# Kernel tuning notes

Measured on AMD Instinct MI355X. Metric: run time of the kernel, lower is better.

## Reference

```python
import jax, jax.numpy as jnp
import numpy as np

N = 50000   # n_nodes
E = 800000  # n_edges (avg degree 16)
D = 128     # d_model == hidden_dim
N_LAYERS = 3


def _xavier(key, fan_in, fan_out):
    limit = float(np.sqrt(6.0 / (fan_in + fan_out)))
    return jax.random.uniform(key, (fan_in, fan_out), jnp.float32, -limit, limit)


def setup_inputs() -> dict:
    key = jax.random.key(0)
    ks = jax.random.split(key, 2 + 2 * N_LAYERS)
    x = jax.random.normal(ks[0], (N, D), jnp.float32)
    edge_index = jax.random.randint(ks[1], (2, E), 0, N, jnp.int32)
    inp = {"x": x, "edge_index": edge_index}
    for i in range(N_LAYERS):
        inp[f"W{i}"] = _xavier(ks[2 + 2 * i], D, D)
        inp[f"b{i}"] = jax.random.uniform(ks[3 + 2 * i], (D,), jnp.float32, -0.1, 0.1)
    return inp


def _gcn_forward(x, src, dst, norm, Ws, bs):
    n = x.shape[0]
    h = x
    for i, (W, b) in enumerate(zip(Ws, bs)):
        m = (h @ W)[src] * norm[:, None]                       # [E+N, D] gather + scale
        h = jax.ops.segment_sum(m, dst, num_segments=n) + b    # scatter-add aggregate
        if i < len(Ws) - 1:
            h = jax.nn.relu(h)
    return h + x                                               # residual


def reference(x, edge_index, W0, b0, W1, b1, W2, b2):
    n = x.shape[0]
    loop = jnp.arange(n, dtype=edge_index.dtype)
    src = jnp.concatenate([edge_index[0], loop])  # add self-loops (GCNConv default)
    dst = jnp.concatenate([edge_index[1], loop])
    deg = jax.ops.segment_sum(jnp.ones_like(dst, x.dtype), dst, num_segments=n)
    dinv = jax.lax.rsqrt(deg)                     # deg >= 1 due to self-loops
    norm = dinv[src] * dinv[dst]                  # symmetric GCN normalization
    return _gcn_forward(x, src, dst, norm, (W0, W1, W2), (b0, b1, b2))
```

## Files before the change

kernel.cpp:

```cpp
#include <hip/hip_runtime.h>
#include <hip/hip_bf16.h>

#define D 128
#define BCAP 64
#define TM 64
#define TMF 32


__device__ __forceinline__ unsigned short f2bf_rtne(float f) {
    unsigned int u = __float_as_uint(f);
    u += 0x7fffu + ((u >> 16) & 1u);
    return (unsigned short)(u >> 16);
}

__device__ __forceinline__ float bf_lo(unsigned int u) { return __uint_as_float(u << 16); }
__device__ __forceinline__ float bf_hi(unsigned int u) { return __uint_as_float(u & 0xffff0000u); }


__device__ __forceinline__ void gemm_compute64(const float* __restrict__ sh,
                                               const float* __restrict__ W,
                                               unsigned short* __restrict__ out,
                                               const int* __restrict__ cnt,
                                               int n, int nbase) {
    const int tid = threadIdx.x;
    const int c4 = (tid & 31) << 2;
    const int ng = tid >> 5;
    const float* shb = &sh[(ng * 8) * D];

    float4 acc[8];
#pragma unroll
    for (int j = 0; j < 8; ++j) acc[j] = make_float4(0.f, 0.f, 0.f, 0.f);

    for (int k = 0; k < D; k += 4) {
        float4 w0 = *(const float4*)&W[(size_t)(k + 0) * D + c4];
        float4 w1 = *(const float4*)&W[(size_t)(k + 1) * D + c4];
        float4 w2 = *(const float4*)&W[(size_t)(k + 2) * D + c4];
        float4 w3 = *(const float4*)&W[(size_t)(k + 3) * D + c4];
#pragma unroll
        for (int j = 0; j < 8; ++j) {
            float4 hv = *(const float4*)&shb[j * D + k];
            acc[j].x = fmaf(hv.x, w0.x, acc[j].x); acc[j].y = fmaf(hv.x, w0.y, acc[j].y);
            acc[j].z = fmaf(hv.x, w0.z, acc[j].z); acc[j].w = fmaf(hv.x, w0.w, acc[j].w);
            acc[j].x = fmaf(hv.y, w1.x, acc[j].x); acc[j].y = fmaf(hv.y, w1.y, acc[j].y);
            acc[j].z = fmaf(hv.y, w1.z, acc[j].z); acc[j].w = fmaf(hv.y, w1.w, acc[j].w);
            acc[j].x = fmaf(hv.z, w2.x, acc[j].x); acc[j].y = fmaf(hv.z, w2.y, acc[j].y);
            acc[j].z = fmaf(hv.z, w2.z, acc[j].z); acc[j].w = fmaf(hv.z, w2.w, acc[j].w);
            acc[j].x = fmaf(hv.w, w3.x, acc[j].x); acc[j].y = fmaf(hv.w, w3.y, acc[j].y);
            acc[j].z = fmaf(hv.w, w3.z, acc[j].z); acc[j].w = fmaf(hv.w, w3.w, acc[j].w);
        }
    }

#pragma unroll
    for (int j = 0; j < 8; ++j) {
        int node = nbase + ng * 8 + j;
        if (node < n) {
            float sc = 1.0f;
            if (cnt) sc = rsqrtf((float)cnt[node] + 1.0f);
            ushort4 p;
            p.x = f2bf_rtne(acc[j].x * sc);
            p.y = f2bf_rtne(acc[j].y * sc);
            p.z = f2bf_rtne(acc[j].z * sc);
            p.w = f2bf_rtne(acc[j].w * sc);
            *(ushort4*)&out[(size_t)node * D + c4] = p;
        }
    }
}


__global__ __launch_bounds__(256) void fused_gemm0_fill_kernel(
        const float* __restrict__ x, const float* __restrict__ W0,
        unsigned short* __restrict__ A,
        const int* __restrict__ src, const int* __restrict__ dst,
        int* __restrict__ cnt, unsigned short* __restrict__ bucket,
        int n, int E, int r, int gemmB, int fillB) {
    __shared__ float sh[TMF * D];
    int b = blockIdx.x;
    if (b % r == 0) {
        int g = b / r;
        if (g >= gemmB) return;
        const int tid = threadIdx.x;
        const int nbase = g * TMF;
#pragma unroll
        for (int i = 0; i < 4; ++i) {
            int fi = tid + i * 256;
            int node = nbase + (fi >> 5);
            float4 v = make_float4(0.f, 0.f, 0.f, 0.f);
            if (node < n) v = *(const float4*)&x[(size_t)node * D + ((fi & 31) << 2)];
            *(float4*)&sh[fi << 2] = v;
        }
        __syncthreads();

        const int c4 = (tid & 31) << 2;
        const int ng = tid >> 5;
        const float* shb = &sh[(ng * 4) * D];
        float4 acc[4];
#pragma unroll
        for (int j = 0; j < 4; ++j) acc[j] = make_float4(0.f, 0.f, 0.f, 0.f);

        for (int k = 0; k < D; k += 4) {
            float4 w0 = *(const float4*)&W0[(size_t)(k + 0) * D + c4];
            float4 w1 = *(const float4*)&W0[(size_t)(k + 1) * D + c4];
            float4 w2 = *(const float4*)&W0[(size_t)(k + 2) * D + c4];
            float4 w3 = *(const float4*)&W0[(size_t)(k + 3) * D + c4];
#pragma unroll
            for (int j = 0; j < 4; ++j) {
                float4 hv = *(const float4*)&shb[j * D + k];
                acc[j].x = fmaf(hv.x, w0.x, acc[j].x); acc[j].y = fmaf(hv.x, w0.y, acc[j].y);
                acc[j].z = fmaf(hv.x, w0.z, acc[j].z); acc[j].w = fmaf(hv.x, w0.w, acc[j].w);
                acc[j].x = fmaf(hv.y, w1.x, acc[j].x); acc[j].y = fmaf(hv.y, w1.y, acc[j].y);
                acc[j].z = fmaf(hv.y, w1.z, acc[j].z); acc[j].w = fmaf(hv.y, w1.w, acc[j].w);
                acc[j].x = fmaf(hv.z, w2.x, acc[j].x); acc[j].y = fmaf(hv.z, w2.y, acc[j].y);
                acc[j].z = fmaf(hv.z, w2.z, acc[j].z); acc[j].w = fmaf(hv.z, w2.w, acc[j].w);
                acc[j].x = fmaf(hv.w, w3.x, acc[j].x); acc[j].y = fmaf(hv.w, w3.y, acc[j].y);
                acc[j].z = fmaf(hv.w, w3.z, acc[j].z); acc[j].w = fmaf(hv.w, w3.w, acc[j].w);
            }
        }

#pragma unroll
        for (int j = 0; j < 4; ++j) {
            int node = nbase + ng * 4 + j;
            if (node < n) {
                ushort4 p;
                p.x = f2bf_rtne(acc[j].x);
                p.y = f2bf_rtne(acc[j].y);
                p.z = f2bf_rtne(acc[j].z);
                p.w = f2bf_rtne(acc[j].w);
                *(ushort4*)&A[(size_t)node * D + c4] = p;
            }
        }
    } else {
        int fid = b - b / r - 1;
        if (fid >= fillB) return;
        int e = fid * 256 + threadIdx.x;
        if (e >= E) return;
        int s = src[e];
        int d = dst[e];
        int pos = atomicAdd(&cnt[d], 1);
        if (pos < BCAP) bucket[((size_t)d << 6) + pos] = (unsigned short)s;
    }
}


__global__ __launch_bounds__(256) void gemm128_scaled_kernel(
        const unsigned short* __restrict__ h, const float* __restrict__ W,
        unsigned short* __restrict__ out, const int* __restrict__ cnt, int n) {
    __shared__ float sh[TM * D];
    const int tid = threadIdx.x;
    const int nbase = blockIdx.x * TM;
#pragma unroll
    for (int i = 0; i < 8; ++i) {
        int fi = tid + i * 256;
        int node = nbase + (fi >> 5);
        float4 v = make_float4(0.f, 0.f, 0.f, 0.f);
        if (node < n) {
            ushort4 u = *(const ushort4*)&h[(size_t)node * D + ((fi & 31) << 2)];
            v.x = __uint_as_float((unsigned)u.x << 16);
            v.y = __uint_as_float((unsigned)u.y << 16);
            v.z = __uint_as_float((unsigned)u.z << 16);
            v.w = __uint_as_float((unsigned)u.w << 16);
        }
        *(float4*)&sh[fi << 2] = v;
    }
    __syncthreads();
    gemm_compute64(sh, W, out, cnt, n, nbase);
}


__global__ __launch_bounds__(256) void gather_kernel(
        const int* __restrict__ cnt, const unsigned short* __restrict__ bucket,
        const unsigned short* __restrict__ hW, const float* __restrict__ bias,
        const float* __restrict__ x, float* __restrict__ out_f32,
        unsigned short* __restrict__ out_bf16, int n, int scaled_in, int final_layer) {
    int node = blockIdx.x * 8 + (threadIdx.x >> 5);
    if (node >= n) return;
    const int f = (threadIdx.x & 31) << 2;
    const unsigned short* row = bucket + ((size_t)node << 6);
    int len = cnt[node];
    float di = rsqrtf((float)len + 1.0f);
    if (len > BCAP) len = BCAP;
    const int len8 = len & ~7;

    float4 acc0 = make_float4(0.f, 0.f, 0.f, 0.f);
    float4 acc1 = make_float4(0.f, 0.f, 0.f, 0.f);
    int k = 0;
    if (len8 > 0) {
        uint4 pp = *(const uint4*)row;
        if (scaled_in) {
            for (; k < len8; k += 8) {
                uint4 cur = pp;
                pp = *(const uint4*)(row + k + 8);
                int s0 = cur.x & 0xffff, s1 = cur.x >> 16;
                int s2 = cur.y & 0xffff, s3 = cur.y >> 16;
                int s4 = cur.z & 0xffff, s5 = cur.z >> 16;
                int s6 = cur.w & 0xffff, s7 = cur.w >> 16;
                uint2 u0 = *(const uint2*)&hW[(size_t)s0 * D + f];
                uint2 u1 = *(const uint2*)&hW[(size_t)s1 * D + f];
                uint2 u2 = *(const uint2*)&hW[(size_t)s2 * D + f];
                uint2 u3 = *(const uint2*)&hW[(size_t)s3 * D + f];
                uint2 u4 = *(const uint2*)&hW[(size_t)s4 * D + f];
                uint2 u5 = *(const uint2*)&hW[(size_t)s5 * D + f];
                uint2 u6 = *(const uint2*)&hW[(size_t)s6 * D + f];
                uint2 u7 = *(const uint2*)&hW[(size_t)s7 * D + f];
                acc0.x += bf_lo(u0.x); acc0.y += bf_hi(u0.x); acc0.z += bf_lo(u0.y); acc0.w += bf_hi(u0.y);
                acc1.x += bf_lo(u1.x); acc1.y += bf_hi(u1.x); acc1.z += bf_lo(u1.y); acc1.w += bf_hi(u1.y);
                acc0.x += bf_lo(u2.x); acc0.y += bf_hi(u2.x); acc0.z += bf_lo(u2.y); acc0.w += bf_hi(u2.y);
                acc1.x += bf_lo(u3.x); acc1.y += bf_hi(u3.x); acc1.z += bf_lo(u3.y); acc1.w += bf_hi(u3.y);
                acc0.x += bf_lo(u4.x); acc0.y += bf_hi(u4.x); acc0.z += bf_lo(u4.y); acc0.w += bf_hi(u4.y);
                acc1.x += bf_lo(u5.x); acc1.y += bf_hi(u5.x); acc1.z += bf_lo(u5.y); acc1.w += bf_hi(u5.y);
                acc0.x += bf_lo(u6.x); acc0.y += bf_hi(u6.x); acc0.z += bf_lo(u6.y); acc0.w += bf_hi(u6.y);
                acc1.x += bf_lo(u7.x); acc1.y += bf_hi(u7.x); acc1.z += bf_lo(u7.y); acc1.w += bf_hi(u7.y);
            }
        } else {
            for (; k < len8; k += 8) {
                uint4 cur = pp;
                pp = *(const uint4*)(row + k + 8);
                int s0 = cur.x & 0xffff, s1 = cur.x >> 16;
                int s2 = cur.y & 0xffff, s3 = cur.y >> 16;
                int s4 = cur.z & 0xffff, s5 = cur.z >> 16;
                int s6 = cur.w & 0xffff, s7 = cur.w >> 16;
                float n0 = rsqrtf((float)cnt[s0] + 1.0f);
                float n1 = rsqrtf((float)cnt[s1] + 1.0f);
                float n2 = rsqrtf((float)cnt[s2] + 1.0f);
                float n3 = rsqrtf((float)cnt[s3] + 1.0f);
                float n4 = rsqrtf((float)cnt[s4] + 1.0f);
                float n5 = rsqrtf((float)cnt[s5] + 1.0f);
                float n6 = rsqrtf((float)cnt[s6] + 1.0f);
                float n7 = rsqrtf((float)cnt[s7] + 1.0f);
                uint2 u0 = *(const uint2*)&hW[(size_t)s0 * D + f];
                uint2 u1 = *(const uint2*)&hW[(size_t)s1 * D + f];
                uint2 u2 = *(const uint2*)&hW[(size_t)s2 * D + f];
                uint2 u3 = *(const uint2*)&hW[(size_t)s3 * D + f];
                uint2 u4 = *(const uint2*)&hW[(size_t)s4 * D + f];
                uint2 u5 = *(const uint2*)&hW[(size_t)s5 * D + f];
                uint2 u6 = *(const uint2*)&hW[(size_t)s6 * D + f];
                uint2 u7 = *(const uint2*)&hW[(size_t)s7 * D + f];
                acc0.x = fmaf(bf_lo(u0.x), n0, acc0.x); acc0.y = fmaf(bf_hi(u0.x), n0, acc0.y);
                acc0.z = fmaf(bf_lo(u0.y), n0, acc0.z); acc0.w = fmaf(bf_hi(u0.y), n0, acc0.w);
                acc1.x = fmaf(bf_lo(u1.x), n1, acc1.x); acc1.y = fmaf(bf_hi(u1.x), n1, acc1.y);
                acc1.z = fmaf(bf_lo(u1.y), n1, acc1.z); acc1.w = fmaf(bf_hi(u1.y), n1, acc1.w);
                acc0.x = fmaf(bf_lo(u2.x), n2, acc0.x); acc0.y = fmaf(bf_hi(u2.x), n2, acc0.y);
                acc0.z = fmaf(bf_lo(u2.y), n2, acc0.z); acc0.w = fmaf(bf_hi(u2.y), n2, acc0.w);
                acc1.x = fmaf(bf_lo(u3.x), n3, acc1.x); acc1.y = fmaf(bf_hi(u3.x), n3, acc1.y);
                acc1.z = fmaf(bf_lo(u3.y), n3, acc1.z); acc1.w = fmaf(bf_hi(u3.y), n3, acc1.w);
                acc0.x = fmaf(bf_lo(u4.x), n4, acc0.x); acc0.y = fmaf(bf_hi(u4.x), n4, acc0.y);
                acc0.z = fmaf(bf_lo(u4.y), n4, acc0.z); acc0.w = fmaf(bf_hi(u4.y), n4, acc0.w);
                acc1.x = fmaf(bf_lo(u5.x), n5, acc1.x); acc1.y = fmaf(bf_hi(u5.x), n5, acc1.y);
                acc1.z = fmaf(bf_lo(u5.y), n5, acc1.z); acc1.w = fmaf(bf_hi(u5.y), n5, acc1.w);
                acc0.x = fmaf(bf_lo(u6.x), n6, acc0.x); acc0.y = fmaf(bf_hi(u6.x), n6, acc0.y);
                acc0.z = fmaf(bf_lo(u6.y), n6, acc0.z); acc0.w = fmaf(bf_hi(u6.y), n6, acc0.w);
                acc1.x = fmaf(bf_lo(u7.x), n7, acc1.x); acc1.y = fmaf(bf_hi(u7.x), n7, acc1.y);
                acc1.z = fmaf(bf_lo(u7.y), n7, acc1.z); acc1.w = fmaf(bf_hi(u7.y), n7, acc1.w);
            }
        }
    }
    for (; k < len; ++k) {
        int s = row[k];
        float ns = scaled_in ? 1.0f : rsqrtf((float)cnt[s] + 1.0f);
        uint2 u = *(const uint2*)&hW[(size_t)s * D + f];
        acc0.x = fmaf(bf_lo(u.x), ns, acc0.x); acc0.y = fmaf(bf_hi(u.x), ns, acc0.y);
        acc0.z = fmaf(bf_lo(u.y), ns, acc0.z); acc0.w = fmaf(bf_hi(u.y), ns, acc0.w);
    }

    uint2 uh = *(const uint2*)&hW[(size_t)node * D + f];
    float sf = scaled_in ? 1.0f : di;
    float4 acc;
    acc.x = fmaf(bf_lo(uh.x), sf, acc0.x + acc1.x);
    acc.y = fmaf(bf_hi(uh.x), sf, acc0.y + acc1.y);
    acc.z = fmaf(bf_lo(uh.y), sf, acc0.z + acc1.z);
    acc.w = fmaf(bf_hi(uh.y), sf, acc0.w + acc1.w);

    float4 bv = *(const float4*)&bias[f];
    float4 r;
    r.x = fmaf(acc.x, di, bv.x);
    r.y = fmaf(acc.y, di, bv.y);
    r.z = fmaf(acc.z, di, bv.z);
    r.w = fmaf(acc.w, di, bv.w);

    if (final_layer) {
        float4 xv = *(const float4*)&x[(size_t)node * D + f];
        r.x += xv.x; r.y += xv.y; r.z += xv.z; r.w += xv.w;
        *(float4*)&out_f32[(size_t)node * D + f] = r;
    } else {
        ushort4 p;
        p.x = f2bf_rtne(fmaxf(r.x, 0.f));
        p.y = f2bf_rtne(fmaxf(r.y, 0.f));
        p.z = f2bf_rtne(fmaxf(r.z, 0.f));
        p.w = f2bf_rtne(fmaxf(r.w, 0.f));
        *(ushort4*)&out_bf16[(size_t)node * D + f] = p;
    }
}


extern "C" void kernel_launch(void* const* d_in, const int* in_sizes, int n_in,
                              void* d_out, int out_size, void* d_ws, size_t ws_size,
                              hipStream_t stream) {
    const float* x  = (const float*)d_in[0];
    const int*   ei = (const int*)d_in[1];
    const float* Ws[3] = {(const float*)d_in[2], (const float*)d_in[4], (const float*)d_in[6]};
    const float* bs[3] = {(const float*)d_in[3], (const float*)d_in[5], (const float*)d_in[7]};
    float* out = (float*)d_out;

    const int N = in_sizes[0] / D;
    const int E = in_sizes[1] / 2;
    const int* src = ei;
    const int* dst = ei + E;

    char* wsb = (char*)d_ws;
    size_t off = 0;
    int* cnt = (int*)(wsb + off);               off += (size_t)N * sizeof(int);
    off = (off + 255) & ~(size_t)255;
    unsigned short* bucket = (unsigned short*)(wsb + off);  off += (size_t)N * BCAP * 2;
    off = (off + 255) & ~(size_t)255;
    unsigned short* A  = (unsigned short*)(wsb + off);      off += (size_t)N * D * 2;
    off = (off + 255) & ~(size_t)255;
    unsigned short* B  = (unsigned short*)(wsb + off);

    const int gemmBF = (N + TMF - 1) / TMF;
    const int gemmB  = (N + TM - 1) / TM;
    const int fillB = (E + 255) / 256;
    const int r = 1 + (fillB + gemmBF - 1) / gemmBF;
    const int fusedGrid = gemmBF * r;
    const int gatherGrid = (N + 7) / 8;

    hipMemsetAsync(cnt, 0, (size_t)N * sizeof(int), stream);
    fused_gemm0_fill_kernel<<<fusedGrid, 256, 0, stream>>>(x, Ws[0], A, src, dst,
                                                           cnt, bucket, N, E, r, gemmBF, fillB);
    gather_kernel<<<gatherGrid, 256, 0, stream>>>(cnt, bucket, A, bs[0], x, out, B, N, 0, 0);
    gemm128_scaled_kernel<<<gemmB, 256, 0, stream>>>(B, Ws[1], A, cnt, N);
    gather_kernel<<<gatherGrid, 256, 0, stream>>>(cnt, bucket, A, bs[1], x, out, B, N, 1, 0);
    gemm128_scaled_kernel<<<gemmB, 256, 0, stream>>>(B, Ws[2], A, cnt, N);
    gather_kernel<<<gatherGrid, 256, 0, stream>>>(cnt, bucket, A, bs[2], x, out, B, N, 1, 1);
}
```

Baseline: 325.3 us.

## Fuse neighbor aggregation with next-layer GEMM and enlarge first GEMM tile

Layer 0 and 1 aggregation now writes the activated rows of 32 nodes into shared memory and multiplies them by the next weight matrix in the same kernel. This removes the bf16 intermediate round trip through global memory and two kernel launches. It double-buffers the hW arrays (A/A2) because a block reads gathered neighbor rows from other blocks. The first fused GEMM+fill kernel also goes from 32 to 64 nodes per GEMM block. In exchange, the fused kernel has fewer threads gathering per node-tile and may have different occupancy from the extra shared memory.

```diff
diff --git a/kernel.cpp b/kernel.cpp
--- a/kernel.cpp
+++ b/kernel.cpp
@@ -4,7 +4,7 @@
 #define D 128
 #define BCAP 64
 #define TM 64
-#define TMF 32
+#define TG 32
 
 
 __device__ __forceinline__ unsigned short f2bf_rtne(float f) {
@@ -17,163 +17,11 @@
 __device__ __forceinline__ float bf_hi(unsigned int u) { return __uint_as_float(u & 0xffff0000u); }
 
 
-__device__ __forceinline__ void gemm_compute64(const float* __restrict__ sh,
-                                               const float* __restrict__ W,
-                                               unsigned short* __restrict__ out,
-                                               const int* __restrict__ cnt,
-                                               int n, int nbase) {
-    const int tid = threadIdx.x;
-    const int c4 = (tid & 31) << 2;
-    const int ng = tid >> 5;
-    const float* shb = &sh[(ng * 8) * D];
-
-    float4 acc[8];
-#pragma unroll
-    for (int j = 0; j < 8; ++j) acc[j] = make_float4(0.f, 0.f, 0.f, 0.f);
-
-    for (int k = 0; k < D; k += 4) {
-        float4 w0 = *(const float4*)&W[(size_t)(k + 0) * D + c4];
-        float4 w1 = *(const float4*)&W[(size_t)(k + 1) * D + c4];
-        float4 w2 = *(const float4*)&W[(size_t)(k + 2) * D + c4];
-        float4 w3 = *(const float4*)&W[(size_t)(k + 3) * D + c4];
-#pragma unroll
-        for (int j = 0; j < 8; ++j) {
-            float4 hv = *(const float4*)&shb[j * D + k];
-            acc[j].x = fmaf(hv.x, w0.x, acc[j].x); acc[j].y = fmaf(hv.x, w0.y, acc[j].y);
-            acc[j].z = fmaf(hv.x, w0.z, acc[j].z); acc[j].w = fmaf(hv.x, w0.w, acc[j].w);
-            acc[j].x = fmaf(hv.y, w1.x, acc[j].x); acc[j].y = fmaf(hv.y, w1.y, acc[j].y);
-            acc[j].z = fmaf(hv.y, w1.z, acc[j].z); acc[j].w = fmaf(hv.y, w1.w, acc[j].w);
-            acc[j].x = fmaf(hv.z, w2.x, acc[j].x); acc[j].y = fmaf(hv.z, w2.y, acc[j].y);
-            acc[j].z = fmaf(hv.z, w2.z, acc[j].z); acc[j].w = fmaf(hv.z, w2.w, acc[j].w);
-            acc[j].x = fmaf(hv.w, w3.x, acc[j].x); acc[j].y = fmaf(hv.w, w3.y, acc[j].y);
-            acc[j].z = fmaf(hv.w, w3.z, acc[j].z); acc[j].w = fmaf(hv.w, w3.w, acc[j].w);
-        }
-    }
-
-#pragma unroll
-    for (int j = 0; j < 8; ++j) {
-        int node = nbase + ng * 8 + j;
-        if (node < n) {
-            float sc = 1.0f;
-            if (cnt) sc = rsqrtf((float)cnt[node] + 1.0f);
-            ushort4 p;
-            p.x = f2bf_rtne(acc[j].x * sc);
-            p.y = f2bf_rtne(acc[j].y * sc);
-            p.z = f2bf_rtne(acc[j].z * sc);
-            p.w = f2bf_rtne(acc[j].w * sc);
-            *(ushort4*)&out[(size_t)node * D + c4] = p;
-        }
-    }
-}
-
-
-__global__ __launch_bounds__(256) void fused_gemm0_fill_kernel(
-        const float* __restrict__ x, const float* __restrict__ W0,
-        unsigned short* __restrict__ A,
-        const int* __restrict__ src, const int* __restrict__ dst,
-        int* __restrict__ cnt, unsigned short* __restrict__ bucket,
-        int n, int E, int r, int gemmB, int fillB) {
-    __shared__ float sh[TMF * D];
-    int b = blockIdx.x;
-    if (b % r == 0) {
-        int g = b / r;
-        if (g >= gemmB) return;
-        const int tid = threadIdx.x;
-        const int nbase = g * TMF;
-#pragma unroll
-        for (int i = 0; i < 4; ++i) {
-            int fi = tid + i * 256;
-            int node = nbase + (fi >> 5);
-            float4 v = make_float4(0.f, 0.f, 0.f, 0.f);
-            if (node < n) v = *(const float4*)&x[(size_t)node * D + ((fi & 31) << 2)];
-            *(float4*)&sh[fi << 2] = v;
-        }
-        __syncthreads();
-
-        const int c4 = (tid & 31) << 2;
-        const int ng = tid >> 5;
-        const float* shb = &sh[(ng * 4) * D];
-        float4 acc[4];
-#pragma unroll
-        for (int j = 0; j < 4; ++j) acc[j] = make_float4(0.f, 0.f, 0.f, 0.f);
-
-        for (int k = 0; k < D; k += 4) {
-            float4 w0 = *(const float4*)&W0[(size_t)(k + 0) * D + c4];
-            float4 w1 = *(const float4*)&W0[(size_t)(k + 1) * D + c4];
-            float4 w2 = *(const float4*)&W0[(size_t)(k + 2) * D + c4];
-            float4 w3 = *(const float4*)&W0[(size_t)(k + 3) * D + c4];
-#pragma unroll
-            for (int j = 0; j < 4; ++j) {
-                float4 hv = *(const float4*)&shb[j * D + k];
-                acc[j].x = fmaf(hv.x, w0.x, acc[j].x); acc[j].y = fmaf(hv.x, w0.y, acc[j].y);
-                acc[j].z = fmaf(hv.x, w0.z, acc[j].z); acc[j].w = fmaf(hv.x, w0.w, acc[j].w);
-                acc[j].x = fmaf(hv.y, w1.x, acc[j].x); acc[j].y = fmaf(hv.y, w1.y, acc[j].y);
-                acc[j].z = fmaf(hv.y, w1.z, acc[j].z); acc[j].w = fmaf(hv.y, w1.w, acc[j].w);
-                acc[j].x = fmaf(hv.z, w2.x, acc[j].x); acc[j].y = fmaf(hv.z, w2.y, acc[j].y);
-                acc[j].z = fmaf(hv.z, w2.z, acc[j].z); acc[j].w = fmaf(hv.z, w2.w, acc[j].w);
-                acc[j].x = fmaf(hv.w, w3.x, acc[j].x); acc[j].y = fmaf(hv.w, w3.y, acc[j].y);
-                acc[j].z = fmaf(hv.w, w3.z, acc[j].z); acc[j].w = fmaf(hv.w, w3.w, acc[j].w);
-            }
-        }
-
-#pragma unroll
-        for (int j = 0; j < 4; ++j) {
-            int node = nbase + ng * 4 + j;
-            if (node < n) {
-                ushort4 p;
-                p.x = f2bf_rtne(acc[j].x);
-                p.y = f2bf_rtne(acc[j].y);
-                p.z = f2bf_rtne(acc[j].z);
-                p.w = f2bf_rtne(acc[j].w);
-                *(ushort4*)&A[(size_t)node * D + c4] = p;
-            }
-        }
-    } else {
-        int fid = b - b / r - 1;
-        if (fid >= fillB) return;
-        int e = fid * 256 + threadIdx.x;
-        if (e >= E) return;
-        int s = src[e];
-        int d = dst[e];
-        int pos = atomicAdd(&cnt[d], 1);
-        if (pos < BCAP) bucket[((size_t)d << 6) + pos] = (unsigned short)s;
-    }
-}
-
-
-__global__ __launch_bounds__(256) void gemm128_scaled_kernel(
-        const unsigned short* __restrict__ h, const float* __restrict__ W,
-        unsigned short* __restrict__ out, const int* __restrict__ cnt, int n) {
-    __shared__ float sh[TM * D];
-    const int tid = threadIdx.x;
-    const int nbase = blockIdx.x * TM;
-#pragma unroll
-    for (int i = 0; i < 8; ++i) {
-        int fi = tid + i * 256;
-        int node = nbase + (fi >> 5);
-        float4 v = make_float4(0.f, 0.f, 0.f, 0.f);
-        if (node < n) {
-            ushort4 u = *(const ushort4*)&h[(size_t)node * D + ((fi & 31) << 2)];
-            v.x = __uint_as_float((unsigned)u.x << 16);
-            v.y = __uint_as_float((unsigned)u.y << 16);
-            v.z = __uint_as_float((unsigned)u.z << 16);
-            v.w = __uint_as_float((unsigned)u.w << 16);
-        }
-        *(float4*)&sh[fi << 2] = v;
-    }
-    __syncthreads();
-    gemm_compute64(sh, W, out, cnt, n, nbase);
-}
-
-
-__global__ __launch_bounds__(256) void gather_kernel(
-        const int* __restrict__ cnt, const unsigned short* __restrict__ bucket,
-        const unsigned short* __restrict__ hW, const float* __restrict__ bias,
-        const float* __restrict__ x, float* __restrict__ out_f32,
-        unsigned short* __restrict__ out_bf16, int n, int scaled_in, int final_layer) {
-    int node = blockIdx.x * 8 + (threadIdx.x >> 5);
-    if (node >= n) return;
-    const int f = (threadIdx.x & 31) << 2;
+__device__ __forceinline__ float4 aggregate_row(const int* __restrict__ cnt,
+                                                const unsigned short* __restrict__ bucket,
+                                                const unsigned short* __restrict__ hW,
+                                                const float* __restrict__ bias,
+                                                int node, int f, int scaled_in) {
     const unsigned short* row = bucket + ((size_t)node << 6);
     int len = cnt[node];
     float di = rsqrtf((float)len + 1.0f);
@@ -275,19 +123,163 @@
     r.y = fmaf(acc.y, di, bv.y);
     r.z = fmaf(acc.z, di, bv.z);
     r.w = fmaf(acc.w, di, bv.w);
-
-    if (final_layer) {
-        float4 xv = *(const float4*)&x[(size_t)node * D + f];
-        r.x += xv.x; r.y += xv.y; r.z += xv.z; r.w += xv.w;
-        *(float4*)&out_f32[(size_t)node * D + f] = r;
+    return r;
+}
+
+
+__global__ __launch_bounds__(256) void fused_gemm0_fill_kernel(
+        const float* __restrict__ x, const float* __restrict__ W0,
+        unsigned short* __restrict__ A,
+        const int* __restrict__ src, const int* __restrict__ dst,
+        int* __restrict__ cnt, unsigned short* __restrict__ bucket,
+        int n, int E, int r, int gemmB, int fillB) {
+    __shared__ float sh[TM * D];
+    int b = blockIdx.x;
+    if (b % r == 0) {
+        int g = b / r;
+        if (g >= gemmB) return;
+        const int tid = threadIdx.x;
+        const int nbase = g * TM;
+#pragma unroll
+        for (int i = 0; i < 8; ++i) {
+            int fi = tid + i * 256;
+            int node = nbase + (fi >> 5);
+            float4 v = make_float4(0.f, 0.f, 0.f, 0.f);
+            if (node < n) v = *(const float4*)&x[(size_t)node * D + ((fi & 31) << 2)];
+            *(float4*)&sh[fi << 2] = v;
+        }
+        __syncthreads();
+
+        const int c4 = (tid & 31) << 2;
+        const int ng = tid >> 5;
+        const float* shb = &sh[(ng * 8) * D];
+        float4 acc[8];
+#pragma unroll
+        for (int j = 0; j < 8; ++j) acc[j] = make_float4(0.f, 0.f, 0.f, 0.f);
+
+        for (int k = 0; k < D; k += 4) {
+            float4 w0 = *(const float4*)&W0[(size_t)(k + 0) * D + c4];
+            float4 w1 = *(const float4*)&W0[(size_t)(k + 1) * D + c4];
+            float4 w2 = *(const float4*)&W0[(size_t)(k + 2) * D + c4];
+            float4 w3 = *(const float4*)&W0[(size_t)(k + 3) * D + c4];
+#pragma unroll
+            for (int j = 0; j < 8; ++j) {
+                float4 hv = *(const float4*)&shb[j * D + k];
+                acc[j].x = fmaf(hv.x, w0.x, acc[j].x); acc[j].y = fmaf(hv.x, w0.y, acc[j].y);
+                acc[j].z = fmaf(hv.x, w0.z, acc[j].z); acc[j].w = fmaf(hv.x, w0.w, acc[j].w);
+                acc[j].x = fmaf(hv.y, w1.x, acc[j].x); acc[j].y = fmaf(hv.y, w1.y, acc[j].y);
+                acc[j].z = fmaf(hv.y, w1.z, acc[j].z); acc[j].w = fmaf(hv.y, w1.w, acc[j].w);
+                acc[j].x = fmaf(hv.z, w2.x, acc[j].x); acc[j].y = fmaf(hv.z, w2.y, acc[j].y);
+                acc[j].z = fmaf(hv.z, w2.z, acc[j].z); acc[j].w = fmaf(hv.z, w2.w, acc[j].w);
+                acc[j].x = fmaf(hv.w, w3.x, acc[j].x); acc[j].y = fmaf(hv.w, w3.y, acc[j].y);
+                acc[j].z = fmaf(hv.w, w3.z, acc[j].z); acc[j].w = fmaf(hv.w, w3.w, acc[j].w);
+            }
+        }
+
+#pragma unroll
+        for (int j = 0; j < 8; ++j) {
+            int node = nbase + ng * 8 + j;
+            if (node < n) {
+                ushort4 p;
+                p.x = f2bf_rtne(acc[j].x);
+                p.y = f2bf_rtne(acc[j].y);
+                p.z = f2bf_rtne(acc[j].z);
+                p.w = f2bf_rtne(acc[j].w);
+                *(ushort4*)&A[(size_t)node * D + c4] = p;
+            }
+        }
     } else {
-        ushort4 p;
-        p.x = f2bf_rtne(fmaxf(r.x, 0.f));
-        p.y = f2bf_rtne(fmaxf(r.y, 0.f));
-        p.z = f2bf_rtne(fmaxf(r.z, 0.f));
-        p.w = f2bf_rtne(fmaxf(r.w, 0.f));
-        *(ushort4*)&out_bf16[(size_t)node * D + f] = p;
-    }
+        int fid = b - b / r - 1;
+        if (fid >= fillB) return;
+        int e = fid * 256 + threadIdx.x;
+        if (e >= E) return;
+        int s = src[e];
+        int d = dst[e];
+        int pos = atomicAdd(&cnt[d], 1);
+        if (pos < BCAP) bucket[((size_t)d << 6) + pos] = (unsigned short)s;
+    }
+}
+
+
+__global__ __launch_bounds__(256) void fused_gather_gemm_kernel(
+        const int* __restrict__ cnt, const unsigned short* __restrict__ bucket,
+        const unsigned short* __restrict__ hW_in, const float* __restrict__ bias,
+        const float* __restrict__ W, unsigned short* __restrict__ hW_out,
+        int n, int scaled_in) {
+    __shared__ float sh[TG * D];
+    const int nbase = blockIdx.x * TG;
+    const int g = threadIdx.x >> 5;
+    const int f = (threadIdx.x & 31) << 2;
+
+#pragma unroll
+    for (int j = 0; j < 4; ++j) {
+        int nl = g * 4 + j;
+        int node = nbase + nl;
+        float4 r = make_float4(0.f, 0.f, 0.f, 0.f);
+        if (node < n) {
+            r = aggregate_row(cnt, bucket, hW_in, bias, node, f, scaled_in);
+            r.x = fmaxf(r.x, 0.f);
+            r.y = fmaxf(r.y, 0.f);
+            r.z = fmaxf(r.z, 0.f);
+            r.w = fmaxf(r.w, 0.f);
+        }
+        *(float4*)&sh[nl * D + f] = r;
+    }
+    __syncthreads();
+
+    const int c4 = (threadIdx.x & 31) << 2;
+    const int ng = threadIdx.x >> 5;
+    const float* shb = &sh[(ng * 4) * D];
+    float4 acc[4];
+#pragma unroll
+    for (int j = 0; j < 4; ++j) acc[j] = make_float4(0.f, 0.f, 0.f, 0.f);
+
+    for (int k = 0; k < D; k += 4) {
+        float4 w0 = *(const float4*)&W[(size_t)(k + 0) * D + c4];
+        float4 w1 = *(const float4*)&W[(size_t)(k + 1) * D + c4];
+        float4 w2 = *(const float4*)&W[(size_t)(k + 2) * D + c4];
+        float4 w3 = *(const float4*)&W[(size_t)(k + 3) * D + c4];
+#pragma unroll
+        for (int j = 0; j < 4; ++j) {
+            float4 hv = *(const float4*)&shb[j * D + k];
+            acc[j].x = fmaf(hv.x, w0.x, acc[j].x); acc[j].y = fmaf(hv.x, w0.y, acc[j].y);
+            acc[j].z = fmaf(hv.x, w0.z, acc[j].z); acc[j].w = fmaf(hv.x, w0.w, acc[j].w);
+            acc[j].x = fmaf(hv.y, w1.x, acc[j].x); acc[j].y = fmaf(hv.y, w1.y, acc[j].y);
+            acc[j].z = fmaf(hv.y, w1.z, acc[j].z); acc[j].w = fmaf(hv.y, w1.w, acc[j].w);
+            acc[j].x = fmaf(hv.z, w2.x, acc[j].x); acc[j].y = fmaf(hv.z, w2.y, acc[j].y);
+            acc[j].z = fmaf(hv.z, w2.z, acc[j].z); acc[j].w = fmaf(hv.z, w2.w, acc[j].w);
+            acc[j].x = fmaf(hv.w, w3.x, acc[j].x); acc[j].y = fmaf(hv.w, w3.y, acc[j].y);
+            acc[j].z = fmaf(hv.w, w3.z, acc[j].z); acc[j].w = fmaf(hv.w, w3.w, acc[j].w);
+        }
+    }
+
+#pragma unroll
+    for (int j = 0; j < 4; ++j) {
+        int node = nbase + ng * 4 + j;
+        if (node < n) {
+            float sc = rsqrtf((float)cnt[node] + 1.0f);
+            ushort4 p;
+            p.x = f2bf_rtne(acc[j].x * sc);
+            p.y = f2bf_rtne(acc[j].y * sc);
+            p.z = f2bf_rtne(acc[j].z * sc);
+            p.w = f2bf_rtne(acc[j].w * sc);
+            *(ushort4*)&hW_out[(size_t)node * D + c4] = p;
+        }
+    }
+}
+
+
+__global__ __launch_bounds__(256) void gather_final_kernel(
+        const int* __restrict__ cnt, const unsigned short* __restrict__ bucket,
+        const unsigned short* __restrict__ hW, const float* __restrict__ bias,
+        const float* __restrict__ x, float* __restrict__ out, int n) {
+    int node = blockIdx.x * 8 + (threadIdx.x >> 5);
+    if (node >= n) return;
+    const int f = (threadIdx.x & 31) << 2;
+    float4 r = aggregate_row(cnt, bucket, hW, bias, node, f, 1);
+    float4 xv = *(const float4*)&x[(size_t)node * D + f];
+    r.x += xv.x; r.y += xv.y; r.z += xv.z; r.w += xv.w;
+    *(float4*)&out[(size_t)node * D + f] = r;
 }
 
 
@@ -313,21 +305,19 @@
     off = (off + 255) & ~(size_t)255;
     unsigned short* A  = (unsigned short*)(wsb + off);      off += (size_t)N * D * 2;
     off = (off + 255) & ~(size_t)255;
-    unsigned short* B  = (unsigned short*)(wsb + off);
-
-    const int gemmBF = (N + TMF - 1) / TMF;
-    const int gemmB  = (N + TM - 1) / TM;
+    unsigned short* A2 = (unsigned short*)(wsb + off);
+
+    const int gemmB = (N + TM - 1) / TM;
     const int fillB = (E + 255) / 256;
-    const int r = 1 + (fillB + gemmBF - 1) / gemmBF;
-    const int fusedGrid = gemmBF * r;
+    const int r = 1 + (fillB + gemmB - 1) / gemmB;
+    const int fusedGrid = gemmB * r;
+    const int ggGrid = (N + TG - 1) / TG;
     const int gatherGrid = (N + 7) / 8;
 
     hipMemsetAsync(cnt, 0, (size_t)N * sizeof(int), stream);
     fused_gemm0_fill_kernel<<<fusedGrid, 256, 0, stream>>>(x, Ws[0], A, src, dst,
-                                                           cnt, bucket, N, E, r, gemmBF, fillB);
-    gather_kernel<<<gatherGrid, 256, 0, stream>>>(cnt, bucket, A, bs[0], x, out, B, N, 0, 0);
-    gemm128_scaled_kernel<<<gemmB, 256, 0, stream>>>(B, Ws[1], A, cnt, N);
-    gather_kernel<<<gatherGrid, 256, 0, stream>>>(cnt, bucket, A, bs[1], x, out, B, N, 1, 0);
-    gemm128_scaled_kernel<<<gemmB, 256, 0, stream>>>(B, Ws[2], A, cnt, N);
-    gather_kernel<<<gatherGrid, 256, 0, stream>>>(cnt, bucket, A, bs[2], x, out, B, N, 1, 1);
-}
+                                                           cnt, bucket, N, E, r, gemmB, fillB);
+    fused_gather_gemm_kernel<<<ggGrid, 256, 0, stream>>>(cnt, bucket, A, bs[0], Ws[1], A2, N, 0);
+    fused_gather_gemm_kernel<<<ggGrid, 256, 0, stream>>>(cnt, bucket, A2, bs[1], Ws[2], A, N, 1);
+    gather_final_kernel<<<gatherGrid, 256, 0, stream>>>(cnt, bucket, A, bs[2], x, out, N);
+}
```

Result: slower. 335.6 us (+3.2%).
